# Optimization experiments

Hardware: AMD Instinct MI355X
Metric: run time of the kernel (lower is better)

The kernel has to match this reference:

```python
import jax, jax.numpy as jnp
import numpy as np

N_NODES = 50000
N_EDGES = 800000
DIM = 128
LN_EPS = 1e-5


def setup_inputs() -> dict:
    key = jax.random.key(0)
    k1, k2, k3, k4 = jax.random.split(key, 4)
    h = jax.random.normal(k1, (N_NODES, DIM), dtype=jnp.float32)
    edge_index = jax.random.randint(k2, (2, N_EDGES), 0, N_NODES, dtype=jnp.int64)
    W = jax.random.normal(k3, (DIM, DIM), dtype=jnp.float32) / np.sqrt(DIM)
    b = jnp.zeros((DIM,), dtype=jnp.float32)
    gamma = jnp.ones((DIM,), dtype=jnp.float32)
    beta = jnp.zeros((DIM,), dtype=jnp.float32)
    t = jnp.zeros((), dtype=jnp.float32)
    return {"t": t, "h": h, "edge_index": edge_index, "batch_size": N_NODES,
            "W": W, "b": b, "gamma": gamma, "beta": beta}


def _gcn_conv(h, edge_index, W, b):
    """PyG-style GCNConv: D^{-1/2} (A+I) D^{-1/2} (h W) + b."""
    N = h.shape[0]
    loops = jnp.arange(N, dtype=edge_index.dtype)
    src = jnp.concatenate([edge_index[0], loops])  # [E+N]
    dst = jnp.concatenate([edge_index[1], loops])  # [E+N]
    # degree (with self loops) on destination nodes
    deg = jax.ops.segment_sum(jnp.ones_like(dst, dtype=h.dtype), dst, num_segments=N)
    dinv = jnp.where(deg > 0, jax.lax.rsqrt(deg), 0.0)
    norm = dinv[src] * dinv[dst]                    # [E+N]
    xw = h @ W                                      # [N, D]
    msg = xw[src] * norm[:, None]                   # gather + scale, [E+N, D]
    agg = jax.ops.segment_sum(msg, dst, num_segments=N)  # scatter-add, [N, D]
    return agg + b


def reference(t, h, edge_index, batch_size, W, b, gamma, beta):
    if h.ndim == 1:
        h = h[None, :]
    dh = _gcn_conv(h, edge_index, W, b)
    # LayerNorm over feature dim, then tanh
    mean = jnp.mean(dh, axis=-1, keepdims=True)
    var = jnp.mean(jnp.square(dh - mean), axis=-1, keepdims=True)
    dh = (dh - mean) * jax.lax.rsqrt(var + LN_EPS) * gamma + beta
    dh = jnp.tanh(dh)
    return (dh, jnp.zeros_like(edge_index), jnp.zeros_like(jnp.asarray(batch_size)))
```

## Files before the change

### kernel.cpp

```cpp
#include <hip/hip_runtime.h>
#include <math.h>

#define NN 50000
#define NE 800000
#define D  128
#define SCAN_CHUNK 1024
#define NSCAN ((NN + SCAN_CHUNK - 1) / SCAN_CHUNK)
#define PG_BLOCKS 782

typedef __attribute__((ext_vector_type(8))) short bf16x8;
typedef __attribute__((ext_vector_type(4))) float f32x4;

__device__ __forceinline__ unsigned short f32_to_bf16(float f) {
    unsigned u = __float_as_uint(f);
    u = u + 0x7FFFu + ((u >> 16) & 1u);
    return (unsigned short)(u >> 16);
}

__device__ __forceinline__ float fast_tanh(float x) {
    float e = __expf(2.0f * x);
    return fmaf(-2.0f, __builtin_amdgcn_rcpf(e + 1.0f), 1.0f);
}

__global__ __launch_bounds__(256) void k_count(
        const float* __restrict__ Wg, const int* __restrict__ ei,
        int* __restrict__ deg, unsigned short* __restrict__ rank,
        unsigned short* __restrict__ wpk, unsigned short* __restrict__ zb,
        int* __restrict__ outtail, int tailN) {
    int tid = threadIdx.x;
    int g = blockIdx.x * 256 + tid;

    if (g < NE / 4) {
        int4 d4 = ((const int4*)(ei + NE))[g];
        ushort4 r;
        r.x = (unsigned short)atomicAdd(&deg[d4.x], 1);
        r.y = (unsigned short)atomicAdd(&deg[d4.y], 1);
        r.z = (unsigned short)atomicAdd(&deg[d4.z], 1);
        r.w = (unsigned short)atomicAdd(&deg[d4.w], 1);
        ((ushort4*)rank)[g] = r;
    }
    for (int i = g; i < tailN; i += PG_BLOCKS * 256) outtail[i] = 0;

    if (blockIdx.x == 0) {
#pragma unroll 8
        for (int i = 0; i < 64; i++) {
            int o = i * 256 + tid;
            int j = o & 7, frag = o >> 3;
            int lo = frag & 15, quad = (frag >> 4) & 3;
            int kt = (frag >> 6) & 3, nt = frag >> 8;
            int k = kt * 32 + quad * 8 + j, n = nt * 16 + lo;
            wpk[o] = f32_to_bf16(Wg[k * 128 + n]);
        }
    }
    if (blockIdx.x == 1 && tid < 64)
        ((unsigned*)(zb + (size_t)NN * D))[tid] = 0u;
}

__global__ __launch_bounds__(256) void k_scan(const int* __restrict__ deg,
                                              int* __restrict__ partial,
                                              int* __restrict__ flag,
                                              int* __restrict__ rowoff,
                                              float* __restrict__ dinv) {
    __shared__ int wsum[4];
    int t = threadIdx.x;
    int bid = blockIdx.x;
    int lane = t & 63, wv = t >> 6;
    int base = bid * SCAN_CHUNK + t * 4;
    int d[4]; int s = 0;
#pragma unroll
    for (int j = 0; j < 4; j++) {
        int i = base + j;
        d[j] = 0;
        if (i < NN) {
            d[j] = deg[i];
            s += d[j];
            dinv[i] = rsqrtf((float)d[j] + 1.0f);
        }
    }
    int v = s;
#pragma unroll
    for (int off = 1; off < 64; off <<= 1) {
        int u = __shfl_up(v, off, 64);
        if (lane >= off) v += u;
    }
    if (lane == 63) wsum[wv] = v;
    __syncthreads();
    int add = 0;
#pragma unroll
    for (int k = 0; k < 4; k++) if (k < wv) add += wsum[k];
    int inc = v + add;

    if (t == 255) {
        atomicExch(&partial[bid], inc);
        __threadfence();
        atomicAdd(flag, 1);
        while (atomicAdd(flag, 0) < NSCAN) {}
    }
    __syncthreads();

    int pv = (lane < NSCAN && lane < bid) ? atomicAdd(&partial[lane], 0) : 0;
#pragma unroll
    for (int off = 32; off > 0; off >>= 1) pv += __shfl_xor(pv, off, 64);

    int ex = inc - s + pv;
#pragma unroll
    for (int j = 0; j < 4; j++) {
        int i = base + j;
        if (i < NN) {
            rowoff[i] = ex;
            ex += d[j];
            if (i == NN - 1) rowoff[NN] = ex;
        }
    }
}

__global__ __launch_bounds__(256) void k_gemm_fill(
        const float* __restrict__ h, const uint4* __restrict__ wpk4,
        const int* __restrict__ ei, const unsigned short* __restrict__ rank,
        const int* __restrict__ rowoff, const float* __restrict__ dinv,
        unsigned short* __restrict__ zb, int* __restrict__ csr) {
    int tid = threadIdx.x;
    int g = blockIdx.x * 256 + tid;

    if (g < NE / 4) {
        int4 s4 = ((const int4*)ei)[g];
        int4 d4 = ((const int4*)(ei + NE))[g];
        ushort4 r4 = ((const ushort4*)rank)[g];
        csr[rowoff[d4.x] + r4.x] = s4.x;
        csr[rowoff[d4.y] + r4.y] = s4.y;
        csr[rowoff[d4.z] + r4.z] = s4.z;
        csr[rowoff[d4.w] + r4.w] = s4.w;
    }

    int w = tid >> 6, lane = tid & 63;
    int quad = lane >> 4, lo = lane & 15;
    int rowBase = blockIdx.x * 64 + w * 16;
    int rowA = rowBase + lo; if (rowA > NN - 1) rowA = NN - 1;
    const float4* h4 = (const float4*)h;

    bf16x8 af[4];
#pragma unroll
    for (int kt = 0; kt < 4; kt++) {
        float4 u = h4[(size_t)rowA * 32 + kt * 8 + quad * 2];
        float4 v = h4[(size_t)rowA * 32 + kt * 8 + quad * 2 + 1];
        bf16x8 a;
        a[0] = (short)f32_to_bf16(u.x); a[1] = (short)f32_to_bf16(u.y);
        a[2] = (short)f32_to_bf16(u.z); a[3] = (short)f32_to_bf16(u.w);
        a[4] = (short)f32_to_bf16(v.x); a[5] = (short)f32_to_bf16(v.y);
        a[6] = (short)f32_to_bf16(v.z); a[7] = (short)f32_to_bf16(v.w);
        af[kt] = a;
    }

    f32x4 acc[8];
#pragma unroll
    for (int nt = 0; nt < 8; nt++) acc[nt] = (f32x4){0.f, 0.f, 0.f, 0.f};

#pragma unroll
    for (int kt = 0; kt < 4; kt++) {
#pragma unroll
        for (int nt = 0; nt < 8; nt++) {
            uint4 tb = wpk4[nt * 256 + kt * 64 + lane];
            bf16x8 bfv = __builtin_bit_cast(bf16x8, tb);
            acc[nt] = __builtin_amdgcn_mfma_f32_16x16x32_bf16(af[kt], bfv, acc[nt], 0, 0, 0);
        }
    }

#pragma unroll
    for (int reg = 0; reg < 4; reg++) {
        int row = rowBase + quad * 4 + reg;
        if (row < NN) {
            float dn = dinv[row];
#pragma unroll
            for (int nt = 0; nt < 8; nt++)
                zb[(size_t)row * D + nt * 16 + lo] = f32_to_bf16(acc[nt][reg] * dn);
        }
    }
}

__global__ __launch_bounds__(256) void k_gather_ln(
        const int* __restrict__ rowoff, const int* __restrict__ csr,
        const float* __restrict__ dinv, const unsigned* __restrict__ zbu,
        const float* __restrict__ bias, const float* __restrict__ gamma,
        const float* __restrict__ beta, float* __restrict__ out) {
    int tid = threadIdx.x;
    int w = tid >> 6, lane = tid & 63;
    int rowBase = blockIdx.x * 16 + w * 4;

    int cs[4], ce[4]; float dn[4]; unsigned selfz[4]; int v0[4];
#pragma unroll
    for (int r = 0; r < 4; r++) {
        int row = rowBase + r;
        cs[r] = __builtin_amdgcn_readfirstlane(rowoff[row]);
        ce[r] = __builtin_amdgcn_readfirstlane(rowoff[row + 1]);
        dn[r] = dinv[row];
        selfz[r] = zbu[(size_t)row * 64 + lane];
    }
#pragma unroll
    for (int r = 0; r < 4; r++) {
        int m0 = ce[r] - cs[r]; if (m0 > 64) m0 = 64;
        int t0 = csr[cs[r] + lane];
        v0[r] = (lane < m0) ? t0 : NN;
    }

    float2 x[4];
#pragma unroll
    for (int r = 0; r < 4; r++) {
        float ax = __uint_as_float(selfz[r] << 16);
        float ay = __uint_as_float(selfz[r] & 0xFFFF0000u);
        int c = cs[r];
        int v = v0[r];
        while (true) {
            int m = ce[r] - c; if (m > 64) m = 64;
            int nb = (m + 15) >> 4;
            for (int jb = 0; jb < nb; ++jb) {
                int j = jb << 4;
                unsigned p[16];
#pragma unroll
                for (int q = 0; q < 16; q++) {
                    int sq = __builtin_amdgcn_readlane(v, j + q);
                    p[q] = zbu[(size_t)sq * 64 + lane];
                }
#pragma unroll
                for (int q = 0; q < 16; q++) {
                    ax += __uint_as_float(p[q] << 16);
                    ay += __uint_as_float(p[q] & 0xFFFF0000u);
                }
            }
            c += 64;
            if (c >= ce[r]) break;
            int m2 = ce[r] - c; if (m2 > 64) m2 = 64;
            int t2 = csr[c + lane];
            v = (lane < m2) ? t2 : NN;
        }
        x[r].x = ax * dn[r];
        x[r].y = ay * dn[r];
    }

    float2 bi = ((const float2*)bias)[lane];
    float2 ga = ((const float2*)gamma)[lane];
    float2 be = ((const float2*)beta)[lane];
#pragma unroll
    for (int r = 0; r < 4; r++) {
        int row = rowBase + r;
        float y0 = x[r].x + bi.x;
        float y1 = x[r].y + bi.y;
        float s = y0 + y1;
#pragma unroll
        for (int off = 32; off > 0; off >>= 1) s += __shfl_xor(s, off, 64);
        float m = s * (1.0f / 128.0f);
        float v0f = y0 - m, v1f = y1 - m;
        float vs = v0f * v0f + v1f * v1f;
#pragma unroll
        for (int off = 32; off > 0; off >>= 1) vs += __shfl_xor(vs, off, 64);
        float rstd = rsqrtf(vs * (1.0f / 128.0f) + 1e-5f);
        float2 o;
        o.x = fast_tanh(v0f * rstd * ga.x + be.x);
        o.y = fast_tanh(v1f * rstd * ga.y + be.y);
        *(float2*)&out[(size_t)row * D + lane * 2] = o;
    }
}

extern "C" void kernel_launch(void* const* d_in, const int* in_sizes, int n_in,
                              void* d_out, int out_size, void* d_ws, size_t ws_size,
                              hipStream_t stream) {
    const float* h     = (const float*)d_in[1];
    const int*   ei    = (const int*)  d_in[2];
    const float* Wg    = (const float*)d_in[4];
    const float* b     = (const float*)d_in[5];
    const float* gamma = (const float*)d_in[6];
    const float* beta  = (const float*)d_in[7];
    float* out = (float*)d_out;

    char* wsb = (char*)d_ws;
    unsigned short* wpk    = (unsigned short*)(wsb);
    int*            deg    = (int*)(wsb + 32768);
    int*            flag   = (int*)(wsb + 232768);
    int*            partial= (int*)(wsb + 232832);
    unsigned short* rank   = (unsigned short*)(wsb + 233088);
    int*            rowoff = (int*)(wsb + 1833088);
    float*          dinv   = (float*)(wsb + 2633152);
    int*            csr    = (int*)(wsb + 2833152);
    unsigned short* zb     = (unsigned short*)(wsb + 6033408);

    int tailN = out_size - NN * D;
    int* outtail = (int*)(out + (size_t)NN * D);

    hipMemsetAsync(deg, 0, NN * sizeof(int) + sizeof(int), stream);
    k_count    <<<PG_BLOCKS, 256, 0, stream>>>(Wg, ei, deg, rank, wpk, zb, outtail, tailN);
    k_scan     <<<NSCAN,     256, 0, stream>>>(deg, partial, flag, rowoff, dinv);
    k_gemm_fill<<<PG_BLOCKS, 256, 0, stream>>>(h, (const uint4*)wpk, ei, rank, rowoff, dinv, zb, csr);
    k_gather_ln<<<NN / 16,   256, 0, stream>>>(rowoff, csr, dinv, (const unsigned*)zb, b, gamma, beta, out);
}
```

Measured before the change: 202.5 us.

## Overlap GEMM with degree counting and defer dinv scaling to fill pass

Replaces the memset with an init kernel that zeros the degree array and packs W. Degree counting and the unscaled GEMM now run in one launch, interleaved as odd and even blocks, so the GEMM no longer waits for the scan. The GEMM writes an fp32 intermediate. A new fill kernel builds the CSR and applies the dinv scale with bf16 conversion. This adds a full fp32 write and read of the 50000x128 intermediate (about 25.6 MB each way) in exchange for moving the GEMM off the critical path after the scan.

```diff
diff --git a/kernel.cpp b/kernel.cpp
--- a/kernel.cpp
+++ b/kernel.cpp
@@ -22,24 +22,14 @@
     return fmaf(-2.0f, __builtin_amdgcn_rcpf(e + 1.0f), 1.0f);
 }
 
-__global__ __launch_bounds__(256) void k_count(
-        const float* __restrict__ Wg, const int* __restrict__ ei,
-        int* __restrict__ deg, unsigned short* __restrict__ rank,
-        unsigned short* __restrict__ wpk, unsigned short* __restrict__ zb,
-        int* __restrict__ outtail, int tailN) {
+__global__ __launch_bounds__(256) void k_init(
+        const float* __restrict__ Wg, int* __restrict__ deg,
+        unsigned short* __restrict__ wpk, unsigned short* __restrict__ zb) {
     int tid = threadIdx.x;
-    int g = blockIdx.x * 256 + tid;
-
-    if (g < NE / 4) {
-        int4 d4 = ((const int4*)(ei + NE))[g];
-        ushort4 r;
-        r.x = (unsigned short)atomicAdd(&deg[d4.x], 1);
-        r.y = (unsigned short)atomicAdd(&deg[d4.y], 1);
-        r.z = (unsigned short)atomicAdd(&deg[d4.z], 1);
-        r.w = (unsigned short)atomicAdd(&deg[d4.w], 1);
-        ((ushort4*)rank)[g] = r;
-    }
-    for (int i = g; i < tailN; i += PG_BLOCKS * 256) outtail[i] = 0;
+    int idx = blockIdx.x * 256 + tid;
+
+    if (idx < 12500) ((int4*)deg)[idx] = (int4){0, 0, 0, 0};
+    if (idx == 12500) deg[50000] = 0;
 
     if (blockIdx.x == 0) {
 #pragma unroll 8
@@ -54,6 +44,74 @@
     }
     if (blockIdx.x == 1 && tid < 64)
         ((unsigned*)(zb + (size_t)NN * D))[tid] = 0u;
+}
+
+__global__ __launch_bounds__(256) void k_count_gemm(
+        const float* __restrict__ h, const uint4* __restrict__ wpk4,
+        const int* __restrict__ ei, int* __restrict__ deg,
+        unsigned short* __restrict__ rank, float* __restrict__ zf,
+        int* __restrict__ outtail, int tailN) {
+    int tid = threadIdx.x;
+    int bid = blockIdx.x;
+
+    if (bid & 1) {
+        int g = (bid >> 1) * 256 + tid;
+        if (g < NE / 4) {
+            int4 d4 = ((const int4*)(ei + NE))[g];
+            ushort4 r;
+            r.x = (unsigned short)atomicAdd(&deg[d4.x], 1);
+            r.y = (unsigned short)atomicAdd(&deg[d4.y], 1);
+            r.z = (unsigned short)atomicAdd(&deg[d4.z], 1);
+            r.w = (unsigned short)atomicAdd(&deg[d4.w], 1);
+            ((ushort4*)rank)[g] = r;
+        }
+        for (int i = g; i < tailN; i += PG_BLOCKS * 256) outtail[i] = 0;
+        return;
+    }
+
+    int gid = bid >> 1;
+    int w = tid >> 6, lane = tid & 63;
+    int quad = lane >> 4, lo = lane & 15;
+    int rowBase = gid * 64 + w * 16;
+    int rowA = rowBase + lo; if (rowA > NN - 1) rowA = NN - 1;
+    const float4* h4 = (const float4*)h;
+
+    bf16x8 af[4];
+#pragma unroll
+    for (int kt = 0; kt < 4; kt++) {
+        float4 u = h4[(size_t)rowA * 32 + kt * 8 + quad * 2];
+        float4 v = h4[(size_t)rowA * 32 + kt * 8 + quad * 2 + 1];
+        bf16x8 a;
+        a[0] = (short)f32_to_bf16(u.x); a[1] = (short)f32_to_bf16(u.y);
+        a[2] = (short)f32_to_bf16(u.z); a[3] = (short)f32_to_bf16(u.w);
+        a[4] = (short)f32_to_bf16(v.x); a[5] = (short)f32_to_bf16(v.y);
+        a[6] = (short)f32_to_bf16(v.z); a[7] = (short)f32_to_bf16(v.w);
+        af[kt] = a;
+    }
+
+    f32x4 acc[8];
+#pragma unroll
+    for (int nt = 0; nt < 8; nt++) acc[nt] = (f32x4){0.f, 0.f, 0.f, 0.f};
+
+#pragma unroll
+    for (int kt = 0; kt < 4; kt++) {
+#pragma unroll
+        for (int nt = 0; nt < 8; nt++) {
+            uint4 tb = wpk4[nt * 256 + kt * 64 + lane];
+            bf16x8 bfv = __builtin_bit_cast(bf16x8, tb);
+            acc[nt] = __builtin_amdgcn_mfma_f32_16x16x32_bf16(af[kt], bfv, acc[nt], 0, 0, 0);
+        }
+    }
+
+#pragma unroll
+    for (int reg = 0; reg < 4; reg++) {
+        int row = rowBase + quad * 4 + reg;
+        if (row < NN) {
+#pragma unroll
+            for (int nt = 0; nt < 8; nt++)
+                zf[(size_t)row * D + nt * 16 + lo] = acc[nt][reg];
+        }
+    }
 }
 
 __global__ __launch_bounds__(256) void k_scan(const int* __restrict__ deg,
@@ -114,66 +172,34 @@
     }
 }
 
-__global__ __launch_bounds__(256) void k_gemm_fill(
-        const float* __restrict__ h, const uint4* __restrict__ wpk4,
-        const int* __restrict__ ei, const unsigned short* __restrict__ rank,
-        const int* __restrict__ rowoff, const float* __restrict__ dinv,
-        unsigned short* __restrict__ zb, int* __restrict__ csr) {
-    int tid = threadIdx.x;
-    int g = blockIdx.x * 256 + tid;
-
-    if (g < NE / 4) {
-        int4 s4 = ((const int4*)ei)[g];
-        int4 d4 = ((const int4*)(ei + NE))[g];
-        ushort4 r4 = ((const ushort4*)rank)[g];
-        csr[rowoff[d4.x] + r4.x] = s4.x;
-        csr[rowoff[d4.y] + r4.y] = s4.y;
-        csr[rowoff[d4.z] + r4.z] = s4.z;
-        csr[rowoff[d4.w] + r4.w] = s4.w;
-    }
-
-    int w = tid >> 6, lane = tid & 63;
-    int quad = lane >> 4, lo = lane & 15;
-    int rowBase = blockIdx.x * 64 + w * 16;
-    int rowA = rowBase + lo; if (rowA > NN - 1) rowA = NN - 1;
-    const float4* h4 = (const float4*)h;
-
-    bf16x8 af[4];
-#pragma unroll
-    for (int kt = 0; kt < 4; kt++) {
-        float4 u = h4[(size_t)rowA * 32 + kt * 8 + quad * 2];
-        float4 v = h4[(size_t)rowA * 32 + kt * 8 + quad * 2 + 1];
-        bf16x8 a;
-        a[0] = (short)f32_to_bf16(u.x); a[1] = (short)f32_to_bf16(u.y);
-        a[2] = (short)f32_to_bf16(u.z); a[3] = (short)f32_to_bf16(u.w);
-        a[4] = (short)f32_to_bf16(v.x); a[5] = (short)f32_to_bf16(v.y);
-        a[6] = (short)f32_to_bf16(v.z); a[7] = (short)f32_to_bf16(v.w);
-        af[kt] = a;
-    }
-
-    f32x4 acc[8];
-#pragma unroll
-    for (int nt = 0; nt < 8; nt++) acc[nt] = (f32x4){0.f, 0.f, 0.f, 0.f};
-
-#pragma unroll
-    for (int kt = 0; kt < 4; kt++) {
-#pragma unroll
-        for (int nt = 0; nt < 8; nt++) {
-            uint4 tb = wpk4[nt * 256 + kt * 64 + lane];
-            bf16x8 bfv = __builtin_bit_cast(bf16x8, tb);
-            acc[nt] = __builtin_amdgcn_mfma_f32_16x16x32_bf16(af[kt], bfv, acc[nt], 0, 0, 0);
-        }
-    }
-
-#pragma unroll
-    for (int reg = 0; reg < 4; reg++) {
-        int row = rowBase + quad * 4 + reg;
-        if (row < NN) {
-            float dn = dinv[row];
-#pragma unroll
-            for (int nt = 0; nt < 8; nt++)
-                zb[(size_t)row * D + nt * 16 + lo] = f32_to_bf16(acc[nt][reg] * dn);
-        }
+__global__ __launch_bounds__(320) void k_fill_scale(
+        const int* __restrict__ ei, const int* __restrict__ rowoff,
+        const unsigned short* __restrict__ rank, int* __restrict__ csr,
+        const float* __restrict__ zf, const float* __restrict__ dinv,
+        unsigned short* __restrict__ zb) {
+    int t = blockIdx.x * 320 + threadIdx.x;
+
+    int4 s4 = ((const int4*)ei)[t];
+    int4 d4 = ((const int4*)(ei + NE))[t];
+    ushort4 r4 = ((const ushort4*)rank)[t];
+    csr[rowoff[d4.x] + r4.x] = s4.x;
+    csr[rowoff[d4.y] + r4.y] = s4.y;
+    csr[rowoff[d4.z] + r4.z] = s4.z;
+    csr[rowoff[d4.w] + r4.w] = s4.w;
+
+    int row = t >> 2, seg = t & 3;
+    float dn = dinv[row];
+    const float4* src = (const float4*)(zf + (size_t)row * D + seg * 32);
+    uint4* dst = (uint4*)(zb + (size_t)row * D + seg * 32);
+#pragma unroll
+    for (int i = 0; i < 4; i++) {
+        float4 a = src[i * 2], b = src[i * 2 + 1];
+        uint4 o;
+        o.x = (unsigned)f32_to_bf16(a.x * dn) | ((unsigned)f32_to_bf16(a.y * dn) << 16);
+        o.y = (unsigned)f32_to_bf16(a.z * dn) | ((unsigned)f32_to_bf16(a.w * dn) << 16);
+        o.z = (unsigned)f32_to_bf16(b.x * dn) | ((unsigned)f32_to_bf16(b.y * dn) << 16);
+        o.w = (unsigned)f32_to_bf16(b.z * dn) | ((unsigned)f32_to_bf16(b.w * dn) << 16);
+        dst[i] = o;
     }
 }
 
@@ -281,13 +307,14 @@
     float*          dinv   = (float*)(wsb + 2633152);
     int*            csr    = (int*)(wsb + 2833152);
     unsigned short* zb     = (unsigned short*)(wsb + 6033408);
+    float*          zf     = (float*)(wsb + 18833664);
 
     int tailN = out_size - NN * D;
     int* outtail = (int*)(out + (size_t)NN * D);
 
-    hipMemsetAsync(deg, 0, NN * sizeof(int) + sizeof(int), stream);
-    k_count    <<<PG_BLOCKS, 256, 0, stream>>>(Wg, ei, deg, rank, wpk, zb, outtail, tailN);
-    k_scan     <<<NSCAN,     256, 0, stream>>>(deg, partial, flag, rowoff, dinv);
-    k_gemm_fill<<<PG_BLOCKS, 256, 0, stream>>>(h, (const uint4*)wpk, ei, rank, rowoff, dinv, zb, csr);
-    k_gather_ln<<<NN / 16,   256, 0, stream>>>(rowoff, csr, dinv, (const unsigned*)zb, b, gamma, beta, out);
-}
+    k_init      <<<64,            256, 0, stream>>>(Wg, deg, wpk, zb);
+    k_count_gemm<<<PG_BLOCKS * 2, 256, 0, stream>>>(h, (const uint4*)wpk, ei, deg, rank, zf, outtail, tailN);
+    k_scan      <<<NSCAN,         256, 0, stream>>>(deg, partial, flag, rowoff, dinv);
+    k_fill_scale<<<625,           320, 0, stream>>>(ei, rowoff, rank, csr, zf, dinv, zb);
+    k_gather_ln <<<NN / 16,       256, 0, stream>>>(rowoff, csr, dinv, (const unsigned*)zb, b, gamma, beta, out);
+}
```

After: 192.5 us. 4.9% less time.
